# Kernel optimization log

Measured on AMD Instinct MI355X. Metric: run time of the kernel, lower is better.

The kernel has to match this reference:

```python
import jax, jax.numpy as jnp
import numpy as np
import math

B, K, Q = 8, 3000, 256
KDIM = QDIM = ADIM = ODIM = 512
H_MA, H_CA = 4, 1
CHUNK = 16
SHARPEN = 1.0
EPS = 1e-6
INIT_R = -4.0


def setup_inputs() -> dict:
    key = jax.random.key(0)
    ks = jax.random.split(key, 10)
    s = 0.02  # weight scale so sigmoid/softmax operate in a sane range
    return {
        "key": jax.random.normal(ks[0], (B, K, KDIM), jnp.float32),
        "query": jax.random.normal(ks[1], (B, Q, QDIM), jnp.float32),
        "w_key_ma": jax.random.normal(ks[2], (KDIM, ADIM), jnp.float32) * s,
        "b_key_ma": jnp.zeros((ADIM,), jnp.float32),
        "w_query_ma": jax.random.normal(ks[3], (QDIM, ADIM), jnp.float32) * s,
        "b_query_ma": jnp.zeros((ADIM,), jnp.float32),
        "r": jnp.full((H_MA,), INIT_R, jnp.float32),
        "w_key_ca": jax.random.normal(ks[4], (KDIM, ADIM), jnp.float32) * s,
        "b_key_ca": jnp.zeros((ADIM,), jnp.float32),
        "w_query_ca": jax.random.normal(ks[5], (QDIM, ADIM), jnp.float32) * s,
        "b_query_ca": jnp.zeros((ADIM,), jnp.float32),
        "w_value": jax.random.normal(ks[6], (KDIM, ODIM), jnp.float32) * s,
        "b_value": jnp.zeros((ODIM,), jnp.float32),
    }


def _heads(x, n_heads):
    # [B, T, n_heads*d] -> [B, n_heads, T, d]
    b, t, d = x.shape
    return x.reshape(b, t, n_heads, d // n_heads).transpose(0, 2, 1, 3)


def moving_sum(x, back, forward):
    """Moving sum over last axis: out[k] = sum_{j=k-back}^{k+forward} x[j].
    Equivalent to F.conv1d with an all-ones kernel (cumsum-difference form)."""
    w = back + forward + 1
    pad = [(0, 0)] * (x.ndim - 1) + [(back, forward)]
    cs = jnp.cumsum(jnp.pad(x, pad), axis=-1)
    cs = jnp.concatenate([jnp.zeros_like(cs[..., :1]), cs], axis=-1)
    return cs[..., w:] - cs[..., :-w]


def exclusive_cumsum(x):
    # [a,b,c] -> [0,a,a+b] along last axis
    z = jnp.zeros_like(x[..., :1])
    return jnp.cumsum(jnp.concatenate([z, x[..., :-1]], axis=-1), axis=-1)


def safe_cumprod(x, eps):
    # exclusive cumprod via cumsum in log space
    return jnp.exp(exclusive_cumsum(jnp.log(jnp.clip(x, eps, 1.0))))


def monotonic_alpha(p_choose, eps):
    """Parallel (training-time) monotonic attention recurrence over qlen.
    p_choose: [B, H, Q, K] -> alpha: [B, H, Q, K]"""
    cp = safe_cumprod(1.0 - p_choose, eps)          # [B,H,Q,K]
    cp_c = jnp.clip(cp, eps, 1.0)
    # scan over query steps
    p_t = jnp.moveaxis(p_choose, 2, 0)              # [Q,B,H,K]
    cp_t = jnp.moveaxis(cp, 2, 0)
    cpc_t = jnp.moveaxis(cp_c, 2, 0)
    b, h, k = p_choose.shape[0], p_choose.shape[1], p_choose.shape[3]
    a0 = jnp.zeros((b, h, k), p_choose.dtype).at[:, :, 0].set(1.0)  # attend to frame 0

    def step(a_prev, inp):
        p_i, cp_i, cpc_i = inp
        a_i = p_i * cp_i * jnp.cumsum(a_prev / cpc_i, axis=-1)
        return a_i, a_i

    _, alpha_t = jax.lax.scan(step, a0, (p_t, cp_t, cpc_t))
    return jnp.moveaxis(alpha_t, 0, 2)              # [B,H,Q,K]


def efficient_chunkwise_attention(alpha, u, chunk_size, sharpening_factor):
    """alpha: [B,H_ma,Q,K], u: [B,H_ca,Q,K] (shared across MA heads).
    Returns beta: [B, H_ma*H_ca, Q, K]."""
    bs, h_ma, qlen, klen = alpha.shape
    a5 = alpha[:, :, None]                          # [B,H_ma,1,Q,K]
    u5 = u[:, None]                                 # [B,1,H_ca,Q,K]
    u5 = u5 - jnp.max(u5, axis=-1, keepdims=True)
    softmax_exp = jnp.clip(jnp.exp(u5), 1e-5, None)
    denom = moving_sum(softmax_exp, back=chunk_size - 1, forward=0)
    beta = softmax_exp * moving_sum(a5 * sharpening_factor / denom,
                                    back=0, forward=chunk_size - 1)
    return beta.reshape(bs, -1, qlen, klen)


def reference(key, query, w_key_ma, b_key_ma, w_query_ma, b_query_ma, r,
              w_key_ca, b_key_ca, w_query_ca, b_query_ca, w_value, b_value):
    scale = math.sqrt(ADIM)
    # monotonic energy (scaled_dot, H_ma heads) + offset r
    k_ma = _heads(key @ w_key_ma + b_key_ma, H_MA)          # [B,H,K,dk]
    q_ma = _heads(query @ w_query_ma + b_query_ma, H_MA)    # [B,H,Q,dk]
    e_ma = jnp.einsum('bhqd,bhkd->bhqk', q_ma, k_ma) / scale
    e_ma = e_ma + r[None, :, None, None]
    p_choose = jax.nn.sigmoid(e_ma)                          # [B,H_ma,Q,K]

    alpha = monotonic_alpha(p_choose, EPS)                   # [B,H_ma,Q,K]

    # chunk energy (scaled_dot, H_ca heads, shared across MA heads)
    k_ca = _heads(key @ w_key_ca + b_key_ca, H_CA)
    q_ca = _heads(query @ w_query_ca + b_query_ca, H_CA)
    u = jnp.einsum('bhqd,bhkd->bhqk', q_ca, k_ca) / scale    # [B,H_ca,Q,K]

    beta = efficient_chunkwise_attention(alpha, u, CHUNK, SHARPEN)  # [B,H_ma,Q,K]

    # context vector
    v = _heads(key @ w_value + b_value, H_MA * H_CA)         # [B,H,K,dv]
    cv = jnp.einsum('bhqk,bhkd->bhqd', beta, v)              # [B,H,Q,dv]
    cv = cv.transpose(0, 2, 1, 3).reshape(B, Q, ODIM)
    return cv, alpha, beta
```

## Files before the change

kernel.cpp:

```cpp
#include <hip/hip_runtime.h>
#include <hip/hip_bf16.h>
#include <math.h>

#define EPSV 1e-6f
#define INV_SCALE 0.04419417382415922f

typedef _Float16 half_t;
typedef __attribute__((ext_vector_type(8))) _Float16 half8;
typedef __attribute__((ext_vector_type(4))) _Float16 half4v;
typedef __attribute__((ext_vector_type(4))) float    f32x4;

__device__ __forceinline__ float ldf(const float* p)  { return *p; }
__device__ __forceinline__ float ldf(const half_t* p) { return (float)*p; }
__device__ __forceinline__ void  stf(float* p, float v)  { *p = v; }
__device__ __forceinline__ void  stf(half_t* p, float v) { *p = (half_t)v; }
__device__ __forceinline__ float frcp(float x) { return __builtin_amdgcn_rcpf(x); }
__device__ __forceinline__ half8 hz8() {
  half8 v = {(_Float16)0,(_Float16)0,(_Float16)0,(_Float16)0,
             (_Float16)0,(_Float16)0,(_Float16)0,(_Float16)0};
  return v;
}

template<int CTRL, int RMASK>
__device__ __forceinline__ float dpp_add_step(float x) {
  int t = __builtin_amdgcn_update_dpp(0, __float_as_int(x), CTRL, RMASK, 0xf, true);
  return x + __int_as_float(t);
}
template<int CTRL, int RMASK>
__device__ __forceinline__ float dpp_mul_step(float x) {
  int t = __builtin_amdgcn_update_dpp(0x3f800000, __float_as_int(x), CTRL, RMASK, 0xf, false);
  return x * __int_as_float(t);
}
__device__ __forceinline__ float wave_iscan_add(float x) {
  x = dpp_add_step<0x111,0xf>(x);
  x = dpp_add_step<0x112,0xf>(x);
  x = dpp_add_step<0x114,0xf>(x);
  x = dpp_add_step<0x118,0xf>(x);
  x = dpp_add_step<0x142,0xa>(x);
  x = dpp_add_step<0x143,0xc>(x);
  return x;
}
__device__ __forceinline__ float wave_iscan_mul(float x) {
  x = dpp_mul_step<0x111,0xf>(x);
  x = dpp_mul_step<0x112,0xf>(x);
  x = dpp_mul_step<0x114,0xf>(x);
  x = dpp_mul_step<0x118,0xf>(x);
  x = dpp_mul_step<0x142,0xa>(x);
  x = dpp_mul_step<0x143,0xc>(x);
  return x;
}

__device__ __forceinline__ void block_sync_lds() {
  asm volatile("s_waitcnt lgkmcnt(0)" ::: "memory");
  __builtin_amdgcn_s_barrier();
  asm volatile("" ::: "memory");
}

__device__ __forceinline__ float cross_sum4(const float* ws, int wid) {
  f32x4 a = *(const f32x4*)ws;
  float s = 0.f;
  #pragma unroll
  for (int j = 0; j < 4; j++) s += (wid > j) ? a[j] : 0.f;
  return s;
}
__device__ __forceinline__ float cross_prod4(const float* ws, int wid) {
  f32x4 a = *(const f32x4*)ws;
  float p = 1.f;
  #pragma unroll
  for (int j = 0; j < 4; j++) p *= (wid > j) ? a[j] : 1.f;
  return p;
}

__global__ __launch_bounds__(256)
void prep(const float* __restrict__ s0, half_t* __restrict__ d0,
          const float* __restrict__ s1, half_t* __restrict__ d1,
          const float* __restrict__ s2, half_t* __restrict__ d2,
          const float* __restrict__ s3, half_t* __restrict__ d3,
          const float* __restrict__ s4, half_t* __restrict__ d4,
          const float* __restrict__ key, half_t* __restrict__ keyh,
          const float* __restrict__ ba, const float* __restrict__ bb,
          const float* __restrict__ bc, const float* __restrict__ bd,
          float* __restrict__ cbq, float* __restrict__ cbk)
{
  __shared__ float t[32][33];
  int blk = blockIdx.x;
  int tid = threadIdx.x;
  if (blk < 1280) {
    const float* W; half_t* WT;
    switch (blk >> 8) {
      case 0: W = s0; WT = d0; break;
      case 1: W = s1; WT = d1; break;
      case 2: W = s2; WT = d2; break;
      case 3: W = s3; WT = d3; break;
      default: W = s4; WT = d4; break;
    }
    int tile = blk & 255;
    int bx = tile & 15, by = tile >> 4;
    int r = tid >> 3, cq = tid & 7;
    float4 v = *(const float4*)&W[(size_t)(bx * 32 + r) * 512 + by * 32 + cq * 4];
    t[r][cq * 4 + 0] = v.x; t[r][cq * 4 + 1] = v.y;
    t[r][cq * 4 + 2] = v.z; t[r][cq * 4 + 3] = v.w;
    __syncthreads();
    half4v o;
    o[0] = (half_t)t[cq * 4 + 0][r];
    o[1] = (half_t)t[cq * 4 + 1][r];
    o[2] = (half_t)t[cq * 4 + 2][r];
    o[3] = (half_t)t[cq * 4 + 3][r];
    *(half4v*)&WT[(size_t)(by * 32 + r) * 512 + bx * 32 + cq * 4] = o;
  } else if (blk < 13280) {
    int i = (blk - 1280) * 256 + tid;
    if (i < 3072000) {
      f32x4 v = *(const f32x4*)&key[(size_t)i * 4];
      half4v h;
      h[0] = (half_t)v[0]; h[1] = (half_t)v[1]; h[2] = (half_t)v[2]; h[3] = (half_t)v[3];
      *(half4v*)&keyh[(size_t)i * 4] = h;
    }
  } else {
    if (cbq != nullptr) {
      for (int i = tid; i < 512; i += 256) {
        cbq[i] = ba[i]; cbq[512 + i] = bb[i];
        cbk[i] = bc[i]; cbk[512 + i] = bd[i];
      }
    }
  }
}

struct GemmLds { half_t As[4][128][8]; half_t Bs[4][128][8]; };
struct __align__(16) ScanLds { float wsA[2][4]; float wsB[2][4]; };

__device__ __forceinline__
void stage_a(GemmLds& L, int tid, const float* __restrict__ A,
             int M, int Ke, int lda, int m0, int k0)
{
  #pragma unroll
  for (int i = 0; i < 4; i++) {
    int ch = tid + i * 256;
    int m = ch >> 3, cq = ch & 7, k = cq * 4;
    float4 v = make_float4(0.f, 0.f, 0.f, 0.f);
    if (m0 + m < M && k0 + k < Ke) v = *(const float4*)&A[(size_t)(m0 + m) * lda + k0 + k];
    half4v h;
    h[0] = (half_t)v.x; h[1] = (half_t)v.y; h[2] = (half_t)v.z; h[3] = (half_t)v.w;
    *(half4v*)&L.As[cq >> 1][m][(cq & 1) * 4] = h;
  }
}
__device__ __forceinline__
void stage_a(GemmLds& L, int tid, const half_t* __restrict__ A,
             int M, int Ke, int lda, int m0, int k0)
{
  #pragma unroll
  for (int i = 0; i < 2; i++) {
    int ch = tid + i * 256;
    int m = ch >> 2, kb = ch & 3;
    half8 v = hz8();
    if (m0 + m < M && k0 + kb * 8 < Ke)
      v = *(const half8*)&A[(size_t)(m0 + m) * lda + k0 + kb * 8];
    *(half8*)&L.As[kb][m][0] = v;
  }
}

template<int MODE, bool CT, bool ATOM, typename TA, typename TC>
__device__ __forceinline__
void mgemm_body(GemmLds& L, int tid, int bxx, int byy, int bzz,
                const TA* __restrict__ A, const half_t* __restrict__ BT,
                TC* __restrict__ C, int M, int N, int Kd,
                int lda, int ldb, int ldc, int hdiv, int kdiv, int kc,
                long long sAb, long long sAh, long long sBb, long long sBh,
                long long sCb, long long sCh,
                const float* __restrict__ bias, const float* __restrict__ rvec)
{
  int ks = bzz % kdiv; int zz = bzz / kdiv;
  int bz = zz / hdiv, hz = zz - bz * hdiv;
  A  += (size_t)bz * sAb + (size_t)hz * sAh + (size_t)ks * kc;
  BT += (size_t)bz * sBb + (size_t)hz * sBh + (size_t)ks * kc;
  C  += (size_t)bz * sCb + (size_t)hz * sCh;
  int Ke = Kd - ks * kc; if (Ke > kc) Ke = kc;

  int lane = tid & 63, wid = tid >> 6;
  int wm = wid >> 1, wn = wid & 1;
  int m0 = byy * 128, n0 = bxx * 128;

  f32x4 acc[4][4] = {};

  for (int k0 = 0; k0 < Ke; k0 += 32) {
    stage_a(L, tid, A, M, Ke, lda, m0, k0);
    #pragma unroll
    for (int i = 0; i < 2; i++) {
      int ch = tid + i * 256;
      int n = ch >> 2, kb = ch & 3;
      half8 v = hz8();
      if (n0 + n < N && k0 + kb * 8 < Ke)
        v = *(const half8*)&BT[(size_t)(n0 + n) * ldb + k0 + kb * 8];
      *(half8*)&L.Bs[kb][n][0] = v;
    }
    __syncthreads();
    int kb = lane >> 4, r = lane & 15;
    half8 af[4], bfv[4];
    #pragma unroll
    for (int mi = 0; mi < 4; mi++) af[mi]  = *(const half8*)&L.As[kb][wm * 64 + mi * 16 + r][0];
    #pragma unroll
    for (int ni = 0; ni < 4; ni++) bfv[ni] = *(const half8*)&L.Bs[kb][wn * 64 + ni * 16 + r][0];
    #pragma unroll
    for (int mi = 0; mi < 4; mi++)
      #pragma unroll
      for (int ni = 0; ni < 4; ni++)
        acc[mi][ni] = __builtin_amdgcn_mfma_f32_16x16x32_f16(af[mi], bfv[ni], acc[mi][ni], 0, 0, 0);
    __syncthreads();
  }

  float radd = (MODE == 1) ? rvec[hz] : 0.f;
  int r = lane & 15, g = lane >> 4;
  #pragma unroll
  for (int mi = 0; mi < 4; mi++) {
    #pragma unroll
    for (int ni = 0; ni < 4; ni++) {
      int col = n0 + wn * 64 + ni * 16 + r;
      if (col >= N) continue;
      float bv = (MODE == 0) ? bias[col] : 0.f;
      if (CT) {
        int row0 = m0 + wm * 64 + mi * 16 + g * 4;
        if (row0 + 3 < M) {
          half4v o;
          #pragma unroll
          for (int j = 0; j < 4; j++) o[j] = (half_t)(acc[mi][ni][j] + bv);
          *(half4v*)&((half_t*)C)[(size_t)col * ldc + row0] = o;
        }
      } else {
        #pragma unroll
        for (int j = 0; j < 4; j++) {
          int row = m0 + wm * 64 + mi * 16 + g * 4 + j;
          if (row >= M) continue;
          float v = acc[mi][ni][j];
          if (MODE == 0)      v += bv;
          else if (MODE == 1) v = frcp(1.f + expf(-(v * INV_SCALE + radd)));
          else if (MODE == 2) v *= INV_SCALE;
          if (ATOM) atomicAdd((float*)&C[(size_t)row * ldc + col], v);
          else      stf(&C[(size_t)row * ldc + col], v);
        }
      }
    }
  }
}

template<int MODE, bool CT, bool ATOM, typename TA, typename TC>
__global__ __launch_bounds__(256)
void mgemm(const TA* __restrict__ A, const half_t* __restrict__ BT,
           TC* __restrict__ C, int M, int N, int Kd,
           int lda, int ldb, int ldc, int hdiv, int kdiv, int kc,
           long long sAb, long long sAh, long long sBb, long long sBh,
           long long sCb, long long sCh,
           const float* __restrict__ bias, const float* __restrict__ rvec)
{
  __shared__ GemmLds L;
  mgemm_body<MODE,CT,ATOM,TA,TC>(L, threadIdx.x, blockIdx.x, blockIdx.y, blockIdx.z,
                                 A, BT, C, M, N, Kd, lda, ldb, ldc, hdiv, kdiv, kc,
                                 sAb, sAh, sBb, sBh, sCb, sCh, bias, rvec);
}

__global__ __launch_bounds__(256)
void qk_fused(const float* __restrict__ query, const half_t* __restrict__ keyh,
              const half_t* __restrict__ wt_q, const half_t* __restrict__ wt_k,
              half_t* __restrict__ qbuf, half_t* __restrict__ kbuf2,
              const float* __restrict__ cb_q, const float* __restrict__ cb_k)
{
  __shared__ GemmLds L;
  int blk = blockIdx.x;
  if (blk < 128) {
    mgemm_body<0,false,false,float,half_t>(L, threadIdx.x, blk & 7, blk >> 3, 0,
        query, wt_q, qbuf, 2048, 1024, 512, 512, 512, 1024, 1, 1, 512,
        0, 0, 0, 0, 0, 0, cb_q, nullptr);
  } else {
    int vb = blk - 128;
    mgemm_body<0,false,false,half_t,half_t>(L, threadIdx.x, vb % 8, vb / 8, 0,
        keyh, wt_k, kbuf2, 24000, 1024, 512, 512, 512, 1024, 1, 1, 512,
        0, 0, 0, 0, 0, 0, cb_k, nullptr);
  }
}

union MidLds { GemmLds g; ScanLds s; };

__global__ __launch_bounds__(256, 1)
void fused_mid(const half_t* __restrict__ p16, float* __restrict__ alpha_slot,
               const half_t* __restrict__ qa, const half_t* __restrict__ kb,
               int lda_u, int ldb_u, long long sAb_u, long long sBb_u,
               float* __restrict__ u_buf,
               const half_t* __restrict__ keyh, const half_t* __restrict__ wt_v,
               half_t* __restrict__ vtbuf, const float* __restrict__ b_value)
{
  __shared__ MidLds lds;
  int blk = blockIdx.x;
  int tid = threadIdx.x;

  if (blk >= 32) {
    if (blk < 416) {
      int vb = blk - 32;
      int bx = vb % 24; int t = vb / 24;
      int by = t & 1;   int bz = t >> 1;
      mgemm_body<2,false,false,half_t,float>(lds.g, tid, bx, by, bz, qa, kb, u_buf,
          256, 3000, 512, lda_u, ldb_u, 3000, 1, 1, 512,
          sAb_u, 0, sBb_u, 0, 768000, 0, nullptr, nullptr);
    } else {
      int vb = blk - 416;
      int bx = vb & 3; int by = vb >> 2;
      mgemm_body<0,true,false,half_t,half_t>(lds.g, tid, bx, by, 0, keyh, wt_v, vtbuf,
          24000, 512, 512, 512, 512, 24000, 1, 1, 512,
          0, 0, 0, 0, 0, 0, b_value, nullptr);
    }
    return;
  }

  __builtin_amdgcn_s_setprio(1);
  float (&wsA)[2][4] = lds.s.wsA;
  float (&wsB)[2][4] = lds.s.wsB;
  int lane = tid & 63, wid = tid >> 6;
  int k0 = tid * 12;
  size_t zbase = (size_t)blk * 768000;
  const half_t* prow = p16 + zbase;

  half4v ph0[3], pb0[3], pb1[3], pb2[3], pb3[3], pb4[3], pb5[3], pb6[3], pb7[3];
  #pragma unroll
  for (int j = 0; j < 3; j++) {
    int k = k0 + j * 4;
    half4v z = {(_Float16)0,(_Float16)0,(_Float16)0,(_Float16)0};
    bool ok = (k + 4 <= 3000);
    ph0[j] = ok ? *(const half4v*)&prow[k]         : z;
    pb0[j] = ok ? *(const half4v*)&prow[3000 + k]  : z;
    pb1[j] = ok ? *(const half4v*)&prow[6000 + k]  : z;
    pb2[j] = ok ? *(const half4v*)&prow[9000 + k]  : z;
    pb3[j] = ok ? *(const half4v*)&prow[12000 + k] : z;
    pb4[j] = ok ? *(const half4v*)&prow[15000 + k] : z;
    pb5[j] = ok ? *(const half4v*)&prow[18000 + k] : z;
    pb6[j] = ok ? *(const half4v*)&prow[21000 + k] : z;
    pb7[j] = ok ? *(const half4v*)&prow[24000 + k] : z;
  }

  float a_prev[12];
  #pragma unroll
  for (int c = 0; c < 12; c++) a_prev[c] = 0.f;
  if (tid == 0) a_prev[0] = 1.f;

  float cpv[12], w[12];
  {
    float l[12], m = 1.f;
    float p0f[12];
    #pragma unroll
    for (int c = 0; c < 12; c++) {
      p0f[c] = (float)ph0[c >> 2][c & 3];
      l[c] = m;
      m *= fmaxf(1.f - p0f[c], EPSV);
    }
    float incl = wave_iscan_mul(m);
    if (lane == 63) wsA[1][wid] = incl;
    float exclw = incl * frcp(fmaxf(m, 1e-30f));
    block_sync_lds();
    float base = exclw * cross_prod4(&wsA[1][0], wid);
    #pragma unroll
    for (int c = 0; c < 12; c++) { cpv[c] = base * l[c]; w[c] = p0f[c] * cpv[c]; }
  }

#define SCAN_STEP(I, BUF)                                                     \
  {                                                                           \
    int par = (I) & 1;                                                        \
    float t_[12], s2 = 0.f;                                                   \
    _Pragma("unroll")                                                         \
    for (int c = 0; c < 12; c++) {                                            \
      s2 = fmaf(a_prev[c], frcp(fmaxf(cpv[c], EPSV)), s2);                    \
      t_[c] = s2;                                                             \
    }                                                                         \
    float incl2 = wave_iscan_add(s2);                                         \
    if (lane == 63) wsB[par][wid] = incl2;                                    \
    float excl2 = incl2 - s2;                                                 \
    float pnf[12], l_[12], m_ = 1.f;                                          \
    _Pragma("unroll")                                                         \
    for (int c = 0; c < 12; c++) {                                            \
      pnf[c] = (float)BUF[c >> 2][c & 3];                                     \
      l_[c] = m_;                                                             \
      m_ *= fmaxf(1.f - pnf[c], EPSV);                                        \
    }                                                                         \
    float incl1 = wave_iscan_mul(m_);                                         \
    if (lane == 63) wsA[par][wid] = incl1;                                    \
    float excl1 = incl1 * frcp(fmaxf(m_, 1e-30f));                            \
    block_sync_lds();                                                         \
    if ((I) + 9 <= 255) {                                                     \
      const half_t* nrow = prow + (size_t)((I) + 9) * 3000;                   \
      _Pragma("unroll")                                                       \
      for (int j = 0; j < 3; j++) {                                           \
        int k = k0 + j * 4;                                                   \
        if (k + 4 <= 3000) BUF[j] = *(const half4v*)&nrow[k];                 \
      }                                                                       \
    }                                                                         \
    __builtin_amdgcn_sched_barrier(0);                                        \
    float off = excl2 + cross_sum4(&wsB[par][0], wid);                        \
    size_t rbase = zbase + (size_t)(I) * 3000;                                \
    _Pragma("unroll")                                                         \
    for (int q4 = 0; q4 < 3; q4++) {                                          \
      f32x4 o;                                                                \
      _Pragma("unroll")                                                       \
      for (int j = 0; j < 4; j++) {                                           \
        int c = q4 * 4 + j;                                                   \
        float an = w[c] * (off + t_[c]);                                      \
        a_prev[c] = an;                                                       \
        o[j] = an;                                                            \
      }                                                                       \
      int k = k0 + q4 * 4;                                                    \
      if (k + 4 <= 3000) *(f32x4*)&alpha_slot[rbase + k] = o;                 \
    }                                                                         \
    float base1 = excl1 * cross_prod4(&wsA[par][0], wid);                     \
    _Pragma("unroll")                                                         \
    for (int c = 0; c < 12; c++) { cpv[c] = base1 * l_[c]; w[c] = pnf[c] * cpv[c]; } \
  }

  for (int i = 0; i < 256; i += 8) {
    SCAN_STEP(i,     pb0);
    SCAN_STEP(i + 1, pb1);
    SCAN_STEP(i + 2, pb2);
    SCAN_STEP(i + 3, pb3);
    SCAN_STEP(i + 4, pb4);
    SCAN_STEP(i + 5, pb5);
    SCAN_STEP(i + 6, pb6);
    SCAN_STEP(i + 7, pb7);
  }
#undef SCAN_STEP
}

__global__ __launch_bounds__(256)
void beta_kernel(const float* __restrict__ ubuf, const float* __restrict__ alpha_slot,
                 float* __restrict__ beta_slot)
{
  __shared__ __align__(16) float se[3008];
  __shared__ __align__(16) float dn[3008];
  __shared__ __align__(16) float tt[3040];
  __shared__ float red[4];
  int bq = blockIdx.x;
  int b = bq >> 8, q = bq & 255;
  int tid = threadIdx.x;
  int lane = tid & 63, wid = tid >> 6;
  int k0 = tid * 12;
  bool act = (k0 < 3000);
  const float* urow = ubuf + (size_t)bq * 3000;
  float lmax = -3.0e38f;
  for (int c = tid; c < 750; c += 256) {
    f32x4 v = *(const f32x4*)&urow[c * 4];
    *(f32x4*)&se[c * 4] = v;
    lmax = fmaxf(lmax, fmaxf(fmaxf(v[0], v[1]), fmaxf(v[2], v[3])));
  }
  #pragma unroll
  for (int d = 32; d > 0; d >>= 1) lmax = fmaxf(lmax, __shfl_xor(lmax, d));
  if (lane == 0) red[wid] = lmax;
  __syncthreads();
  float umax = fmaxf(fmaxf(red[0], red[1]), fmaxf(red[2], red[3]));
  for (int c = tid; c < 750; c += 256) {
    f32x4 v = *(const f32x4*)&se[c * 4];
    #pragma unroll
    for (int j = 0; j < 4; j++) v[j] = fmaxf(expf(v[j] - umax), 1e-5f);
    *(f32x4*)&se[c * 4] = v;
  }
  if (tid < 40) tt[3000 + tid] = 0.f;
  __syncthreads();
  if (act) {
    float sb[27];
    #pragma unroll
    for (int j = 0; j < 27; j++) {
      int idx = k0 - 15 + j;
      sb[j] = (idx >= 0) ? se[idx] : 0.f;
    }
    float wsum = 0.f;
    #pragma unroll
    for (int j = 0; j < 16; j++) wsum += sb[j];
    dn[k0] = wsum;
    #pragma unroll
    for (int j = 1; j < 12; j++) {
      wsum += sb[15 + j] - sb[j - 1];
      dn[k0 + j] = wsum;
    }
  }
  __syncthreads();
  for (int h = 0; h < 4; h++) {
    const float* arow = alpha_slot + ((size_t)((b * 4 + h) * 256 + q)) * 3000;
    for (int c = tid; c < 750; c += 256) {
      f32x4 a = *(const f32x4*)&arow[c * 4];
      f32x4 d = *(const f32x4*)&dn[c * 4];
      f32x4 o;
      #pragma unroll
      for (int j = 0; j < 4; j++) o[j] = a[j] * frcp(d[j]);
      *(f32x4*)&tt[c * 4] = o;
    }
    __syncthreads();
    float* brow = beta_slot + ((size_t)((b * 4 + h) * 256 + q)) * 3000;
    if (act) {
      float tb[28];
      #pragma unroll
      for (int j = 0; j < 28; j++) tb[j] = tt[k0 + j];
      float wv = 0.f;
      #pragma unroll
      for (int j = 0; j < 16; j++) wv += tb[j];
      float outv[12];
      outv[0] = se[k0] * wv;
      #pragma unroll
      for (int j = 1; j < 12; j++) {
        wv += tb[15 + j] - tb[j - 1];
        outv[j] = se[k0 + j] * wv;
      }
      #pragma unroll
      for (int q4 = 0; q4 < 3; q4++) {
        f32x4 o;
        #pragma unroll
        for (int j = 0; j < 4; j++) o[j] = outv[q4 * 4 + j];
        *(f32x4*)&brow[k0 + q4 * 4] = o;
      }
    }
    __syncthreads();
  }
}

extern "C" void kernel_launch(void* const* d_in, const int* in_sizes, int n_in,
                              void* d_out, int out_size, void* d_ws, size_t ws_size,
                              hipStream_t stream)
{
  const float* key        = (const float*)d_in[0];
  const float* query      = (const float*)d_in[1];
  const float* w_key_ma   = (const float*)d_in[2];
  const float* b_key_ma   = (const float*)d_in[3];
  const float* w_query_ma = (const float*)d_in[4];
  const float* b_query_ma = (const float*)d_in[5];
  const float* rvec       = (const float*)d_in[6];
  const float* w_key_ca   = (const float*)d_in[7];
  const float* b_key_ca   = (const float*)d_in[8];
  const float* w_query_ca = (const float*)d_in[9];
  const float* b_query_ca = (const float*)d_in[10];
  const float* w_value    = (const float*)d_in[11];
  const float* b_value    = (const float*)d_in[12];

  float* out       = (float*)d_out;
  float* cv_out    = out;
  float* alpha_out = out + (size_t)1048576;
  float* beta_out  = alpha_out + (size_t)24576000;
  half_t* p16      = (half_t*)beta_out;
  half_t* keyh     = (half_t*)(beta_out + 12288000);

  dim3 blk(256);
  bool v3 = ws_size >= (size_t)109322240;

  hipMemsetAsync(cv_out, 0, (size_t)1048576 * sizeof(float), stream);

  if (v3) {
    half_t* kbuf2 = (half_t*)d_ws;
    half_t* qbuf  = (half_t*)((char*)d_ws + 49152000);
    float*  u_buf = (float*)((char*)d_ws + 57540608);
    half_t* vtbuf = (half_t*)((char*)d_ws + 82116608);
    half_t* wt_q  = (half_t*)((char*)d_ws + 106692608);
    half_t* wt_k  = (half_t*)((char*)d_ws + 107741184);
    half_t* wt_v  = (half_t*)((char*)d_ws + 108789760);
    float*  cb_q  = (float*)((char*)d_ws + 109314048);
    float*  cb_k  = (float*)((char*)d_ws + 109318144);

    prep<<<dim3(13281), blk, 0, stream>>>(
        w_query_ma, wt_q, w_query_ca, wt_q + 262144,
        w_key_ma,   wt_k, w_key_ca,   wt_k + 262144,
        w_value,    wt_v, key, keyh,
        b_query_ma, b_query_ca, b_key_ma, b_key_ca, cb_q, cb_k);

    qk_fused<<<dim3(1632), blk, 0, stream>>>(query, keyh, wt_q, wt_k, qbuf, kbuf2, cb_q, cb_k);

    mgemm<1,false,false,half_t,half_t><<<dim3(24,2,32), blk, 0, stream>>>(qbuf, kbuf2, p16, 256,3000, 128, 1024,1024,3000, 4,1,128,
        262144,128, 3072000,128, 3072000,768000, nullptr, rvec);

    fused_mid<<<dim3(1168), blk, 0, stream>>>(p16, alpha_out,
        qbuf + 512, kbuf2 + 512, 1024, 1024, 262144, 3072000,
        u_buf, keyh, wt_v, vtbuf, b_value);

    beta_kernel<<<dim3(2048), blk, 0, stream>>>(u_buf, alpha_out, beta_out);

    mgemm<3,false,true,float,float><<<dim3(1,2,256), blk, 0, stream>>>(beta_out, vtbuf, cv_out, 256,128,3000, 3000,24000,512, 4,8,384,
        3072000,768000, 3000,3072000, 131072,128, nullptr, nullptr);
  } else {
    if (ws_size < (size_t)55967744) return;
    half_t* kbuf   = (half_t*)d_ws;
    half_t* qbuf   = (half_t*)((char*)d_ws + 24576000);
    float*  u_buf  = (float*)((char*)d_ws + 28770304);
    half_t* wt_qma = (half_t*)((char*)d_ws + 53346304);
    half_t* wt_kma = (half_t*)((char*)d_ws + 53870592);
    half_t* wt_qca = (half_t*)((char*)d_ws + 54394880);
    half_t* wt_kca = (half_t*)((char*)d_ws + 54919168);
    half_t* wt_v   = (half_t*)((char*)d_ws + 55443456);

    prep<<<dim3(13281), blk, 0, stream>>>(
        w_query_ma, wt_qma, w_query_ca, wt_qca,
        w_key_ma,   wt_kma, w_key_ca,   wt_kca,
        w_value,    wt_v, key, keyh,
        nullptr, nullptr, nullptr, nullptr, nullptr, nullptr);

    mgemm<0,false,false,float ,half_t><<<dim3(4,16,1),  blk, 0, stream>>>(query, wt_qma, qbuf, 2048, 512, 512, 512,512,512, 1,1,512, 0,0,0,0,0,0, b_query_ma, nullptr);
    mgemm<0,false,false,half_t,half_t><<<dim3(4,188,1), blk, 0, stream>>>(keyh,  wt_kma, kbuf, 24000,512, 512, 512,512,512, 1,1,512, 0,0,0,0,0,0, b_key_ma,   nullptr);
    mgemm<1,false,false,half_t,half_t><<<dim3(24,2,32), blk, 0, stream>>>(qbuf,  kbuf, p16, 256,3000, 128, 512,512,3000, 4,1,128,
        131072,128, 1536000,128, 3072000,768000, nullptr, rvec);

    mgemm<0,false,false,float ,half_t><<<dim3(4,16,1),  blk, 0, stream>>>(query, wt_qca, qbuf, 2048, 512, 512, 512,512,512, 1,1,512, 0,0,0,0,0,0, b_query_ca, nullptr);
    mgemm<0,false,false,half_t,half_t><<<dim3(4,188,1), blk, 0, stream>>>(keyh,  wt_kca, kbuf, 24000,512, 512, 512,512,512, 1,1,512, 0,0,0,0,0,0, b_key_ca,   nullptr);

    fused_mid<<<dim3(416), blk, 0, stream>>>(p16, alpha_out,
        qbuf, kbuf, 512, 512, 131072, 1536000,
        u_buf, keyh, wt_v, kbuf, b_value);

    mgemm<0,true,false,half_t,half_t><<<dim3(4,188,1), blk, 0, stream>>>(keyh, wt_v, kbuf, 24000,512, 512, 512,512,24000, 1,1,512, 0,0,0,0,0,0, b_value, nullptr);

    beta_kernel<<<dim3(2048), blk, 0, stream>>>(u_buf, alpha_out, beta_out);

    mgemm<3,false,true,float,float><<<dim3(1,2,256), blk, 0, stream>>>(beta_out, kbuf, cv_out, 256,128,3000, 3000,24000,512, 4,8,384,
        3072000,768000, 3000,3072000, 131072,128, nullptr, nullptr);
  }
}
```

Baseline: 429.1 us.

## Fuse energy GEMM into scan kernel with flag-based producer-consumer sync

```diff
diff --git a/kernel.cpp b/kernel.cpp
--- a/kernel.cpp
+++ b/kernel.cpp
@@ -71,6 +71,14 @@
   return p;
 }
 
+__device__ __forceinline__ void wait_flag24(unsigned int* f) {
+  int guard = 0;
+  while (__hip_atomic_load(f, __ATOMIC_ACQUIRE, __HIP_MEMORY_SCOPE_AGENT) < 24u) {
+    __builtin_amdgcn_s_sleep(2);
+    if (++guard > 200000) break;
+  }
+}
+
 __global__ __launch_bounds__(256)
 void prep(const float* __restrict__ s0, half_t* __restrict__ d0,
           const float* __restrict__ s1, half_t* __restrict__ d1,
@@ -80,7 +88,8 @@
           const float* __restrict__ key, half_t* __restrict__ keyh,
           const float* __restrict__ ba, const float* __restrict__ bb,
           const float* __restrict__ bc, const float* __restrict__ bd,
-          float* __restrict__ cbq, float* __restrict__ cbk)
+          float* __restrict__ cbq, float* __restrict__ cbk,
+          float* __restrict__ cvz, unsigned int* __restrict__ flags)
 {
   __shared__ float t[32][33];
   int blk = blockIdx.x;
@@ -115,12 +124,19 @@
       h[0] = (half_t)v[0]; h[1] = (half_t)v[1]; h[2] = (half_t)v[2]; h[3] = (half_t)v[3];
       *(half4v*)&keyh[(size_t)i * 4] = h;
     }
-  } else {
+  } else if (blk == 13280) {
     if (cbq != nullptr) {
       for (int i = tid; i < 512; i += 256) {
         cbq[i] = ba[i]; cbq[512 + i] = bb[i];
         cbk[i] = bc[i]; cbk[512 + i] = bd[i];
       }
+    }
+    if (flags != nullptr && tid < 64) flags[tid] = 0u;
+  } else {
+    int i = (blk - 13281) * 256 + tid;
+    if (i < 262144) {
+      f32x4 z = {0.f, 0.f, 0.f, 0.f};
+      *(f32x4*)&cvz[(size_t)i * 4] = z;
     }
   }
 }
@@ -278,28 +294,47 @@
 
 union MidLds { GemmLds g; ScanLds s; };
 
+template<bool EMA>
 __global__ __launch_bounds__(256, 1)
-void fused_mid(const half_t* __restrict__ p16, float* __restrict__ alpha_slot,
+void fused_mid(half_t* __restrict__ p16, float* __restrict__ alpha_slot,
                const half_t* __restrict__ qa, const half_t* __restrict__ kb,
                int lda_u, int ldb_u, long long sAb_u, long long sBb_u,
                float* __restrict__ u_buf,
                const half_t* __restrict__ keyh, const half_t* __restrict__ wt_v,
-               half_t* __restrict__ vtbuf, const float* __restrict__ b_value)
+               half_t* __restrict__ vtbuf, const float* __restrict__ b_value,
+               const half_t* __restrict__ qfull, const half_t* __restrict__ kfull,
+               const float* __restrict__ rvec, unsigned int* __restrict__ flags)
 {
   __shared__ MidLds lds;
   int blk = blockIdx.x;
   int tid = threadIdx.x;
 
   if (blk >= 32) {
-    if (blk < 416) {
+    if (EMA && blk < 1568) {
       int vb = blk - 32;
+      int bx = vb % 24; int t = vb / 24;
+      int by = t & 1;   int bz = t >> 1;
+      mgemm_body<1,false,false,half_t,half_t>(lds.g, tid, bx, by, bz, qfull, kfull, p16,
+          256, 3000, 128, 1024, 1024, 3000, 4, 1, 128,
+          262144, 128, 3072000, 128, 3072000, 768000, nullptr, rvec);
+      __syncthreads();
+      if (tid == 0) {
+        __threadfence();
+        __hip_atomic_fetch_add(&flags[bz * 2 + by], 1u, __ATOMIC_RELEASE, __HIP_MEMORY_SCOPE_AGENT);
+      }
+      return;
+    }
+    int ubase = EMA ? 1568 : 32;
+    int vbase = EMA ? 1952 : 416;
+    if (blk < vbase) {
+      int vb = blk - ubase;
       int bx = vb % 24; int t = vb / 24;
       int by = t & 1;   int bz = t >> 1;
       mgemm_body<2,false,false,half_t,float>(lds.g, tid, bx, by, bz, qa, kb, u_buf,
           256, 3000, 512, lda_u, ldb_u, 3000, 1, 1, 512,
           sAb_u, 0, sBb_u, 0, 768000, 0, nullptr, nullptr);
     } else {
-      int vb = blk - 416;
+      int vb = blk - vbase;
       int bx = vb & 3; int by = vb >> 2;
       mgemm_body<0,true,false,half_t,half_t>(lds.g, tid, bx, by, 0, keyh, wt_v, vtbuf,
           24000, 512, 512, 512, 512, 24000, 1, 1, 512,
@@ -308,6 +343,10 @@
     return;
   }
 
+  if (EMA) {
+    if (tid == 0) wait_flag24(&flags[blk * 2]);
+    block_sync_lds();
+  }
   __builtin_amdgcn_s_setprio(1);
   float (&wsA)[2][4] = lds.s.wsA;
   float (&wsB)[2][4] = lds.s.wsB;
@@ -410,6 +449,10 @@
   }
 
   for (int i = 0; i < 256; i += 8) {
+    if (EMA && i == 112) {
+      if (tid == 0) wait_flag24(&flags[blk * 2 + 1]);
+      block_sync_lds();
+    }
     SCAN_STEP(i,     pb0);
     SCAN_STEP(i + 1, pb1);
     SCAN_STEP(i + 2, pb2);
@@ -540,8 +583,6 @@
   dim3 blk(256);
   bool v3 = ws_size >= (size_t)109322240;
 
-  hipMemsetAsync(cv_out, 0, (size_t)1048576 * sizeof(float), stream);
-
   if (v3) {
     half_t* kbuf2 = (half_t*)d_ws;
     half_t* qbuf  = (half_t*)((char*)d_ws + 49152000);
@@ -551,22 +592,22 @@
     half_t* wt_k  = (half_t*)((char*)d_ws + 107741184);
     half_t* wt_v  = (half_t*)((char*)d_ws + 108789760);
     float*  cb_q  = (float*)((char*)d_ws + 109314048);
+    unsigned int* flags = (unsigned int*)((char*)d_ws + 109316096);
     float*  cb_k  = (float*)((char*)d_ws + 109318144);
 
-    prep<<<dim3(13281), blk, 0, stream>>>(
+    prep<<<dim3(14305), blk, 0, stream>>>(
         w_query_ma, wt_q, w_query_ca, wt_q + 262144,
         w_key_ma,   wt_k, w_key_ca,   wt_k + 262144,
         w_value,    wt_v, key, keyh,
-        b_query_ma, b_query_ca, b_key_ma, b_key_ca, cb_q, cb_k);
+        b_query_ma, b_query_ca, b_key_ma, b_key_ca, cb_q, cb_k,
+        cv_out, flags);
 
     qk_fused<<<dim3(1632), blk, 0, stream>>>(query, keyh, wt_q, wt_k, qbuf, kbuf2, cb_q, cb_k);
 
-    mgemm<1,false,false,half_t,half_t><<<dim3(24,2,32), blk, 0, stream>>>(qbuf, kbuf2, p16, 256,3000, 128, 1024,1024,3000, 4,1,128,
-        262144,128, 3072000,128, 3072000,768000, nullptr, rvec);
-
-    fused_mid<<<dim3(1168), blk, 0, stream>>>(p16, alpha_out,
+    fused_mid<true><<<dim3(2704), blk, 0, stream>>>(p16, alpha_out,
         qbuf + 512, kbuf2 + 512, 1024, 1024, 262144, 3072000,
-        u_buf, keyh, wt_v, vtbuf, b_value);
+        u_buf, keyh, wt_v, vtbuf, b_value,
+        qbuf, kbuf2, rvec, flags);
 
     beta_kernel<<<dim3(2048), blk, 0, stream>>>(u_buf, alpha_out, beta_out);
 
@@ -583,11 +624,12 @@
     half_t* wt_kca = (half_t*)((char*)d_ws + 54919168);
     half_t* wt_v   = (half_t*)((char*)d_ws + 55443456);
 
-    prep<<<dim3(13281), blk, 0, stream>>>(
+    prep<<<dim3(14305), blk, 0, stream>>>(
         w_query_ma, wt_qma, w_query_ca, wt_qca,
         w_key_ma,   wt_kma, w_key_ca,   wt_kca,
         w_value,    wt_v, key, keyh,
-        nullptr, nullptr, nullptr, nullptr, nullptr, nullptr);
+        nullptr, nullptr, nullptr, nullptr, nullptr, nullptr,
+        cv_out, nullptr);
 
     mgemm<0,false,false,float ,half_t><<<dim3(4,16,1),  blk, 0, stream>>>(query, wt_qma, qbuf, 2048, 512, 512, 512,512,512, 1,1,512, 0,0,0,0,0,0, b_query_ma, nullptr);
     mgemm<0,false,false,half_t,half_t><<<dim3(4,188,1), blk, 0, stream>>>(keyh,  wt_kma, kbuf, 24000,512, 512, 512,512,512, 1,1,512, 0,0,0,0,0,0, b_key_ma,   nullptr);
@@ -597,9 +639,10 @@
     mgemm<0,false,false,float ,half_t><<<dim3(4,16,1),  blk, 0, stream>>>(query, wt_qca, qbuf, 2048, 512, 512, 512,512,512, 1,1,512, 0,0,0,0,0,0, b_query_ca, nullptr);
     mgemm<0,false,false,half_t,half_t><<<dim3(4,188,1), blk, 0, stream>>>(keyh,  wt_kca, kbuf, 24000,512, 512, 512,512,512, 1,1,512, 0,0,0,0,0,0, b_key_ca,   nullptr);
 
-    fused_mid<<<dim3(416), blk, 0, stream>>>(p16, alpha_out,
+    fused_mid<false><<<dim3(416), blk, 0, stream>>>(p16, alpha_out,
         qbuf, kbuf, 512, 512, 131072, 1536000,
-        u_buf, keyh, wt_v, kbuf, b_value);
+        u_buf, keyh, wt_v, kbuf, b_value,
+        nullptr, nullptr, nullptr, nullptr);
 
     mgemm<0,true,false,half_t,half_t><<<dim3(4,188,1), blk, 0, stream>>>(keyh, wt_v, kbuf, 24000,512, 512, 512,512,24000, 1,1,512, 0,0,0,0,0,0, b_value, nullptr);
 
```

Result: slower. 564.0 us (+31.4%).
